# Kernel optimization log

Measured on AMD Instinct MI355X. Metric: run time of the kernel, lower is better.

The kernel has to match this reference:

```python
import jax, jax.numpy as jnp
import numpy as np

S, B, E = 1024, 64, 1024   # src_seq_len, batch, encoder_hidden_size
H, A = 1024, 1024          # decoder hidden, attention dim
EMB, V = 512, 32000        # embedding_dim, output vocab


def setup_inputs() -> dict:
    key = jax.random.key(0)
    ks = jax.random.split(key, 16)
    sd = lambda n: 1.0 / np.sqrt(n)
    u = lambda k, shape, n: jax.random.uniform(k, shape, jnp.float32, -sd(n), sd(n))
    return {
        "prev_y": jax.random.normal(ks[0], (B, EMB), jnp.float32),
        "prev_h": jax.random.normal(ks[1], (1, B, H), jnp.float32),
        "enc_out": jax.random.normal(ks[2], (S, B, E), jnp.float32),
        # attention params
        "U_w": u(ks[3], (A, E), E), "U_b": u(ks[4], (A,), E),
        "W_w": u(ks[5], (A, H), H), "W_b": u(ks[6], (A,), H),
        "v_w": u(ks[7], (1, A), A), "v_b": u(ks[8], (1,), A),
        # combine + GRU + output params
        "Wc_w": u(ks[9], (H, EMB + E), EMB + E), "Wc_b": u(ks[10], (H,), EMB + E),
        "W_ih": u(ks[11], (3 * H, H), H), "W_hh": u(ks[12], (3 * H, H), H),
        "b_ih": u(ks[13], (3 * H,), H), "b_hh": u(ks[14], (3 * H,), H),
        "Wout_w": u(ks[15], (V, H), H), "Wout_b": jnp.zeros((V,), jnp.float32),
        "mask": 768,
    }


def reference(prev_y, prev_h, enc_out, U_w, U_b, W_w, W_b, v_w, v_b,
              Wc_w, Wc_b, W_ih, W_hh, b_ih, b_hh, Wout_w, Wout_b, mask):
    s, b, e = enc_out.shape
    h = prev_h[0]                                     # [B,H]
    # --- additive (Bahdanau) attention with multiplicative 0/1 prefix mask ---
    uh = jnp.einsum('sbe,ae->sba', enc_out, U_w) + U_b  # [S,B,A]
    wq = h @ W_w.T + W_b                                # [B,A]
    scores = (jnp.tanh(uh + wq) @ v_w[0] + v_b[0]).T    # [B,S]
    m = min(int(mask), s)
    mask_vec = (jnp.arange(s) < m).astype(scores.dtype) # [S]
    scores = scores * mask_vec                          # multiply, NOT -inf (faithful)
    attn = jax.nn.softmax(scores, axis=1)               # [B,S]
    ctx = jnp.einsum('bs,sbe->be', attn, enc_out)       # [B,E]
    # --- combine + single GRU step (PyTorch gate order r,z,n) ---
    x = jnp.concatenate([prev_y, ctx], axis=1) @ Wc_w.T + Wc_b  # [B,H]
    gi = x @ W_ih.T + b_ih                              # [B,3H]
    gh = h @ W_hh.T + b_hh
    Hh = h.shape[1]
    r = jax.nn.sigmoid(gi[:, :Hh] + gh[:, :Hh])
    z = jax.nn.sigmoid(gi[:, Hh:2 * Hh] + gh[:, Hh:2 * Hh])
    n = jnp.tanh(gi[:, 2 * Hh:] + r * gh[:, 2 * Hh:])
    h_new = (1.0 - z) * n + z * h                       # [B,H]
    # --- output projection + log-softmax ---
    logits = h_new @ Wout_w.T + Wout_b                  # [B,V]
    dec_output = jax.nn.log_softmax(logits, axis=1)
    return dec_output, h_new[None], attn
```

## Files before the change

### kernel.cpp

```cpp
#include <hip/hip_runtime.h>

typedef float f32x4 __attribute__((ext_vector_type(4)));
typedef short short8 __attribute__((ext_vector_type(8)));
typedef unsigned int u32;

#define SEQ   1024
#define VOCAB 32000

__device__ __forceinline__ unsigned short f2bf(float f){
  union { float f; unsigned u; } v; v.f = f;
  unsigned r = v.u + 0x7FFFu + ((v.u >> 16) & 1u);
  return (unsigned short)(r >> 16);
}
__device__ __forceinline__ unsigned pk2(float a, float b){
  return (unsigned)f2bf(a) | ((unsigned)f2bf(b) << 16);
}
__device__ __forceinline__ float bf2f(unsigned short h){
  union { unsigned u; float f; } v; v.u = ((unsigned)h) << 16; return v.f;
}
__device__ __forceinline__ float tanh_fast(float x){
  float a = fminf(fmaxf(x, -15.f), 15.f);
  float e = __expf(2.f * a);
  return (e - 1.f) / (e + 1.f);
}
__device__ __forceinline__ float sigm(float x){ return 1.f / (1.f + expf(-x)); }

__device__ __forceinline__ void ld4(float4* dst, const float* p){
  const float4* q = (const float4*)p;
  dst[0]=q[0]; dst[1]=q[1]; dst[2]=q[2]; dst[3]=q[3];
}
__device__ __forceinline__ void cvt_store(char* base, int row, int kb0, const float4* f){
  int xs = (row & 7) << 4;
  uint4 u;
  u.x = pk2(f[0].x, f[0].y); u.y = pk2(f[0].z, f[0].w);
  u.z = pk2(f[1].x, f[1].y); u.w = pk2(f[1].z, f[1].w);
  *(uint4*)(base + row*128 + (kb0 ^ xs)) = u;
  u.x = pk2(f[2].x, f[2].y); u.y = pk2(f[2].z, f[2].w);
  u.z = pk2(f[3].x, f[3].y); u.w = pk2(f[3].z, f[3].w);
  *(uint4*)(base + row*128 + ((kb0 + 16) ^ xs)) = u;
}
__device__ __forceinline__ void gload_lds16(const void* g, void* l){
  __builtin_amdgcn_global_load_lds((const __attribute__((address_space(1))) u32*)g,
                                   (__attribute__((address_space(3))) u32*)l, 16, 0, 0);
}

__global__ __launch_bounds__(256)
void convert_all(const float* __restrict__ uw, const float* __restrict__ enc,
                 unsigned short* __restrict__ uwb, unsigned short* __restrict__ encb)
{
  const int UWC = 131072;
  const int TOT = UWC + 8388608;
  int stride = gridDim.x * 256;
  for (int c = blockIdx.x*256 + threadIdx.x; c < TOT; c += stride){
    const float* src; unsigned short* dst;
    if (c < UWC){ src = uw + (size_t)c*8;        dst = uwb + (size_t)c*8; }
    else        { size_t e = (size_t)(c-UWC)*8;  src = enc + e; dst = encb + e; }
    float4 f0 = ((const float4*)src)[0], f1 = ((const float4*)src)[1];
    uint4 u;
    u.x = pk2(f0.x,f0.y); u.y = pk2(f0.z,f0.w);
    u.z = pk2(f1.x,f1.y); u.w = pk2(f1.z,f1.w);
    *(uint4*)dst = u;
  }
}

__global__ __launch_bounds__(256)
void score_gemm_bf16(const unsigned short* __restrict__ encb,
                     const unsigned short* __restrict__ uwb,
                     const float* __restrict__ Ub, const float* __restrict__ vw,
                     const float* __restrict__ wqm, const int* __restrict__ maskp,
                     float* __restrict__ scores_part)
{
  __shared__ char smem[32768];
  int m = *maskp; m = m < 0 ? 0 : (m > SEQ ? SEQ : m);
  int bI = blockIdx.x;
  int mtile = bI & 511, ntile = bI >> 9;
  if (mtile * 2 >= m) return;
  int t = threadIdx.x, lane = t & 63, wid = t >> 6;
  int wm = wid >> 1, wn = wid & 1;

  int cswz = (((lane & 7) ^ (lane >> 3)) << 4);
  const char* pa = (const char*)encb + ((size_t)(mtile*128 + wid*8 + (lane>>3)))*2048 + cswz;
  const char* pb = (const char*)uwb  + ((size_t)(ntile*128 + wid*8 + (lane>>3)))*2048 + cswz;

  int aAddr[4], bAddr[4], aXor[4], bXor[4];
  #pragma unroll
  for (int i = 0; i < 4; ++i){
    int ra = wm*64 + i*16 + (lane & 15);
    aAddr[i] = ra * 128; aXor[i] = (ra & 7) << 4;
    int rb = wn*64 + i*16 + (lane & 15);
    bAddr[i] = rb * 128; bXor[i] = (rb & 7) << 4;
  }
  int klane = (lane >> 4) << 4;

  f32x4 acc[4][4] = {};
  char* bA = smem; char* bB = smem + 16384;

  for (int ks = 0; ks < 16; ++ks){
    __syncthreads();
    #pragma unroll
    for (int i = 0; i < 4; ++i){
      gload_lds16(pa + (size_t)i*65536 + ks*128, bA + (i*4 + wid)*1024);
      gload_lds16(pb + (size_t)i*65536 + ks*128, bB + (i*4 + wid)*1024);
    }
    __syncthreads();
    #pragma unroll
    for (int kk = 0; kk < 2; ++kk){
      short8 af[4], bv[4];
      int kb = kk * 64 + klane;
      #pragma unroll
      for (int i = 0; i < 4; ++i){
        af[i] = *(const short8*)(bA + aAddr[i] + (kb ^ aXor[i]));
        bv[i] = *(const short8*)(bB + bAddr[i] + (kb ^ bXor[i]));
      }
      #pragma unroll
      for (int mi = 0; mi < 4; ++mi)
        #pragma unroll
        for (int ni = 0; ni < 4; ++ni)
          acc[mi][ni] = __builtin_amdgcn_mfma_f32_16x16x32_bf16(af[mi], bv[ni], acc[mi][ni], 0, 0, 0);
    }
  }

  int s_idx = mtile * 2 + wm;
  if (s_idx < m){
    float ubv[4], vwv[4];
    #pragma unroll
    for (int ni = 0; ni < 4; ++ni){
      int nt = ntile*128 + wn*64 + ni*16 + (lane & 15);
      ubv[ni] = Ub[nt]; vwv[ni] = vw[nt];
    }
    #pragma unroll
    for (int mi = 0; mi < 4; ++mi){
      #pragma unroll
      for (int j = 0; j < 4; ++j){
        int b = mi*16 + ((lane >> 4) << 2) + j;
        const float* wqrow = wqm + b * 1024;
        float asum = 0.f;
        #pragma unroll
        for (int ni = 0; ni < 4; ++ni){
          int nt = ntile*128 + wn*64 + ni*16 + (lane & 15);
          float uh = acc[mi][ni][j] + ubv[ni] + wqrow[nt];
          asum += tanh_fast(uh) * vwv[ni];
        }
        asum += __shfl_xor(asum, 1, 64);
        asum += __shfl_xor(asum, 2, 64);
        asum += __shfl_xor(asum, 4, 64);
        asum += __shfl_xor(asum, 8, 64);
        if ((lane & 15) == 0)
          scores_part[(ntile*2 + wn)*65536 + s_idx*64 + b] = asum;
      }
    }
  }
}

__global__ __launch_bounds__(256, 2)
void score_gemm_f32(const float* __restrict__ enc, const float* __restrict__ Uw,
                    const float* __restrict__ Ub, const float* __restrict__ vw,
                    const float* __restrict__ wqm, const int* __restrict__ maskp,
                    float* __restrict__ scores_part)
{
  __shared__ char smem[65536];
  int m = *maskp; m = m < 0 ? 0 : (m > SEQ ? SEQ : m);
  int bI = blockIdx.x;
  int mtile = bI & 511, ntile = bI >> 9;
  if (mtile * 2 >= m) return;
  int row0 = mtile * 128;
  int t = threadIdx.x, lane = t & 63;
  int wid = t >> 6, wm = wid >> 1, wn = wid & 1;
  int srow = t >> 2;
  int sk4 = (t & 3) << 4;
  int kb0 = (t & 3) << 5;

  const float* Ag0 = enc + (size_t)(row0 + srow) * 1024 + sk4;
  const float* Ag1 = Ag0 + 64 * 1024;
  const float* Bg0 = Uw  + (size_t)(ntile * 128 + srow) * 1024 + sk4;
  const float* Bg1 = Bg0 + 64 * 1024;

  float4 fa0[4], fa1[4], fb0[4], fb1[4];
  int aAddr[4], bAddr[4], aXor[4], bXor[4];
  #pragma unroll
  for (int i = 0; i < 4; ++i){
    int ra = wm*64 + i*16 + (lane & 15);
    aAddr[i] = ra * 128; aXor[i] = (ra & 7) << 4;
    int rb = wn*64 + i*16 + (lane & 15);
    bAddr[i] = rb * 128; bXor[i] = (rb & 7) << 4;
  }
  int klane = (lane >> 4) << 4;
  f32x4 acc[4][4] = {};

  ld4(fa0, Ag0); ld4(fa1, Ag1); ld4(fb0, Bg0); ld4(fb1, Bg1);
  {
    char* bA = smem; char* bB = smem + 16384;
    cvt_store(bA, srow,      kb0, fa0);
    cvt_store(bA, srow + 64, kb0, fa1);
    cvt_store(bB, srow,      kb0, fb0);
    cvt_store(bB, srow + 64, kb0, fb1);
  }
  #pragma unroll 2
  for (int ks = 0; ks < 16; ++ks){
    int buf = ks & 1;
    if (ks < 15){
      int ko = (ks + 1) * 64;
      ld4(fa0, Ag0 + ko); ld4(fa1, Ag1 + ko);
      ld4(fb0, Bg0 + ko); ld4(fb1, Bg1 + ko);
    }
    __syncthreads();
    {
      char* bA = smem + buf * 32768;
      char* bB = bA + 16384;
      #pragma unroll
      for (int kk = 0; kk < 2; ++kk){
        short8 af[4], bv[4];
        int kb = kk * 64 + klane;
        #pragma unroll
        for (int i = 0; i < 4; ++i){
          af[i] = *(const short8*)(bA + aAddr[i] + (kb ^ aXor[i]));
          bv[i] = *(const short8*)(bB + bAddr[i] + (kb ^ bXor[i]));
        }
        #pragma unroll
        for (int mi = 0; mi < 4; ++mi)
          #pragma unroll
          for (int ni = 0; ni < 4; ++ni)
            acc[mi][ni] = __builtin_amdgcn_mfma_f32_16x16x32_bf16(af[mi], bv[ni], acc[mi][ni], 0, 0, 0);
      }
    }
    if (ks < 15){
      int nb = buf ^ 1;
      char* bA = smem + nb * 32768; char* bB = bA + 16384;
      cvt_store(bA, srow,      kb0, fa0);
      cvt_store(bA, srow + 64, kb0, fa1);
      cvt_store(bB, srow,      kb0, fb0);
      cvt_store(bB, srow + 64, kb0, fb1);
    }
  }

  int s_idx = mtile * 2 + wm;
  if (s_idx < m){
    float ubv[4], vwv[4];
    #pragma unroll
    for (int ni = 0; ni < 4; ++ni){
      int nt = ntile*128 + wn*64 + ni*16 + (lane & 15);
      ubv[ni] = Ub[nt]; vwv[ni] = vw[nt];
    }
    #pragma unroll
    for (int mi = 0; mi < 4; ++mi){
      #pragma unroll
      for (int j = 0; j < 4; ++j){
        int b = mi*16 + ((lane >> 4) << 2) + j;
        const float* wqrow = wqm + b * 1024;
        float asum = 0.f;
        #pragma unroll
        for (int ni = 0; ni < 4; ++ni){
          int nt = ntile*128 + wn*64 + ni*16 + (lane & 15);
          float uh = acc[mi][ni][j] + ubv[ni] + wqrow[nt];
          asum += tanh_fast(uh) * vwv[ni];
        }
        asum += __shfl_xor(asum, 1, 64);
        asum += __shfl_xor(asum, 2, 64);
        asum += __shfl_xor(asum, 4, 64);
        asum += __shfl_xor(asum, 8, 64);
        if ((lane & 15) == 0)
          scores_part[(ntile*2 + wn)*65536 + s_idx*64 + b] = asum;
      }
    }
  }
}

__global__ __launch_bounds__(256)
void gemm_m64(const float* __restrict__ A, const float* __restrict__ Bw,
              const float* __restrict__ bias, float* __restrict__ C,
              float* __restrict__ Cpart, int N, int K, int stepsPerZ)
{
  __shared__ unsigned short sA[2][64 * 40];
  __shared__ unsigned short sB[2][128 * 40];
  int t = threadIdx.x, lane = t & 63, wid = t >> 6;
  int ntile = blockIdx.x, z = blockIdx.z;
  int arow = t >> 2, ak = (t & 3) * 8;
  int brow = t >> 1, bk = (t & 1) * 16;
  const float* Ap = A + (size_t)arow * K + ak + (size_t)z * stepsPerZ * 32;
  const float* Bp = Bw + (size_t)(ntile * 128 + brow) * K + bk + (size_t)z * stepsPerZ * 32;
  int klane = (lane >> 4) << 4;
  f32x4 acc[4][2] = {};
  float4 a0, a1, b0, b1, b2, b3;

  {
    const float4* pa = (const float4*)Ap;
    a0 = pa[0]; a1 = pa[1];
    const float4* pb = (const float4*)Bp;
    b0 = pb[0]; b1 = pb[1]; b2 = pb[2]; b3 = pb[3];
    uint4 u;
    u.x = pk2(a0.x,a0.y); u.y = pk2(a0.z,a0.w);
    u.z = pk2(a1.x,a1.y); u.w = pk2(a1.z,a1.w);
    *(uint4*)((char*)sA[0] + arow*80 + ak*2) = u;
    u.x = pk2(b0.x,b0.y); u.y = pk2(b0.z,b0.w);
    u.z = pk2(b1.x,b1.y); u.w = pk2(b1.z,b1.w);
    *(uint4*)((char*)sB[0] + brow*80 + bk*2) = u;
    u.x = pk2(b2.x,b2.y); u.y = pk2(b2.z,b2.w);
    u.z = pk2(b3.x,b3.y); u.w = pk2(b3.z,b3.w);
    *(uint4*)((char*)sB[0] + brow*80 + bk*2 + 16) = u;
  }

  for (int ks = 0; ks < stepsPerZ; ++ks){
    int buf = ks & 1;
    if (ks + 1 < stepsPerZ){
      int kg = (ks + 1) * 32;
      const float4* pa = (const float4*)(Ap + kg);
      a0 = pa[0]; a1 = pa[1];
      const float4* pb = (const float4*)(Bp + kg);
      b0 = pb[0]; b1 = pb[1]; b2 = pb[2]; b3 = pb[3];
    }
    __syncthreads();
    {
      short8 af[4], bv[2];
      #pragma unroll
      for (int mi = 0; mi < 4; ++mi)
        af[mi] = *(const short8*)((char*)sA[buf] + (mi*16 + (lane & 15))*80 + klane);
      #pragma unroll
      for (int ni = 0; ni < 2; ++ni)
        bv[ni] = *(const short8*)((char*)sB[buf] + (wid*32 + ni*16 + (lane & 15))*80 + klane);
      #pragma unroll
      for (int mi = 0; mi < 4; ++mi)
        #pragma unroll
        for (int ni = 0; ni < 2; ++ni)
          acc[mi][ni] = __builtin_amdgcn_mfma_f32_16x16x32_bf16(af[mi], bv[ni], acc[mi][ni], 0, 0, 0);
    }
    if (ks + 1 < stepsPerZ){
      int nb = buf ^ 1;
      uint4 u;
      u.x = pk2(a0.x,a0.y); u.y = pk2(a0.z,a0.w);
      u.z = pk2(a1.x,a1.y); u.w = pk2(a1.z,a1.w);
      *(uint4*)((char*)sA[nb] + arow*80 + ak*2) = u;
      u.x = pk2(b0.x,b0.y); u.y = pk2(b0.z,b0.w);
      u.z = pk2(b1.x,b1.y); u.w = pk2(b1.z,b1.w);
      *(uint4*)((char*)sB[nb] + brow*80 + bk*2) = u;
      u.x = pk2(b2.x,b2.y); u.y = pk2(b2.z,b2.w);
      u.z = pk2(b3.x,b3.y); u.w = pk2(b3.z,b3.w);
      *(uint4*)((char*)sB[nb] + brow*80 + bk*2 + 16) = u;
    }
  }

  bool multi = (gridDim.z > 1);
  #pragma unroll
  for (int ni = 0; ni < 2; ++ni){
    int cg = ntile*128 + wid*32 + ni*16 + (lane & 15);
    float bz = (bias && !multi) ? bias[cg] : 0.f;
    #pragma unroll
    for (int mi = 0; mi < 4; ++mi){
      int r0 = mi*16 + ((lane >> 4) << 2);
      #pragma unroll
      for (int j = 0; j < 4; ++j){
        float val = acc[mi][ni][j] + bz;
        if (multi) Cpart[((size_t)z*64 + r0 + j)*N + cg] = val;
        else       C[(size_t)(r0 + j)*N + cg] = val;
      }
    }
  }
}

__global__ __launch_bounds__(256)
void reduce8_bias(const float* __restrict__ part, const float* __restrict__ bias,
                  float* __restrict__ out, int N)
{
  int idx = blockIdx.x*256 + threadIdx.x;
  int r = idx / (N >> 2), c4 = (idx % (N >> 2)) * 4;
  f32x4 acc = *(const f32x4*)(bias + c4);
  #pragma unroll
  for (int z = 0; z < 8; ++z)
    acc += *(const f32x4*)(part + ((size_t)z*64 + r)*N + c4);
  *(f32x4*)(out + (size_t)r*N + c4) = acc;
}

__global__ __launch_bounds__(256)
void softmax_attn(const float* __restrict__ sp, const float* __restrict__ vb,
                  const int* __restrict__ maskp, float* __restrict__ attn)
{
  __shared__ float sb[4];
  int b = blockIdx.x, t = threadIdx.x, lane = t & 63, wid = t >> 6;
  int m = *maskp; m = m < 0 ? 0 : (m > SEQ ? SEQ : m);
  float vb0 = vb[0];
  float v[4]; float mx = -1e30f;
  #pragma unroll
  for (int k = 0; k < 4; ++k){
    int s = t + k * 256;
    float x = 0.f;
    if (s < m){
      float a = 0.f;
      #pragma unroll
      for (int p = 0; p < 16; ++p) a += sp[p*65536 + s*64 + b];
      x = a + vb0;
    }
    v[k] = x; mx = fmaxf(mx, x);
  }
  for (int d = 1; d < 64; d <<= 1) mx = fmaxf(mx, __shfl_xor(mx, d, 64));
  if (lane == 0) sb[wid] = mx;
  __syncthreads();
  mx = fmaxf(fmaxf(sb[0], sb[1]), fmaxf(sb[2], sb[3]));
  float sum = 0.f;
  #pragma unroll
  for (int k = 0; k < 4; ++k){ v[k] = expf(v[k] - mx); sum += v[k]; }
  for (int d = 1; d < 64; d <<= 1) sum += __shfl_xor(sum, d, 64);
  __syncthreads();
  if (lane == 0) sb[wid] = sum;
  __syncthreads();
  sum = sb[0] + sb[1] + sb[2] + sb[3];
  #pragma unroll
  for (int k = 0; k < 4; ++k) attn[b*1024 + t + k*256] = v[k] / sum;
}

__global__ __launch_bounds__(256)
void ctx_bf16(const float* __restrict__ attn, const unsigned short* __restrict__ encb,
              float* __restrict__ ctx_part)
{
  int b = blockIdx.x >> 4, ch = blockIdx.x & 15;
  int t = threadIdx.x;
  __shared__ float a_s[64];
  if (t < 64) a_s[t] = attn[b*1024 + ch*64 + t];
  __syncthreads();
  const unsigned short* base = encb + ((size_t)(ch*64)*64 + b)*1024 + t*4;
  f32x4 acc = {};
  for (int s2 = 0; s2 < 64; ++s2){
    ushort4 vv = *(const ushort4*)(base + (size_t)s2*65536);
    float w = a_s[s2];
    acc.x += w * bf2f(vv.x); acc.y += w * bf2f(vv.y);
    acc.z += w * bf2f(vv.z); acc.w += w * bf2f(vv.w);
  }
  *(f32x4*)(ctx_part + (size_t)(b*16 + ch)*1024 + t*4) = acc;
}

__global__ __launch_bounds__(256)
void ctx_f32(const float* __restrict__ attn, const float* __restrict__ enc,
             float* __restrict__ ctx_part)
{
  int b = blockIdx.x >> 4, ch = blockIdx.x & 15;
  int t = threadIdx.x;
  __shared__ float a_s[64];
  if (t < 64) a_s[t] = attn[b*1024 + ch*64 + t];
  __syncthreads();
  const float* ep = enc + (size_t)(ch * 64) * 65536 + b * 1024 + t * 4;
  f32x4 acc = {};
  for (int s2 = 0; s2 < 64; ++s2){
    f32x4 v = *(const f32x4*)(ep + (size_t)s2 * 65536);
    acc += a_s[s2] * v;
  }
  *(f32x4*)(ctx_part + (size_t)(b*16 + ch)*1024 + t*4) = acc;
}

__global__ __launch_bounds__(256)
void build_xcat(const float* __restrict__ part, const float* __restrict__ py,
                float* __restrict__ xcat)
{
  int b = blockIdx.x, t = threadIdx.x;
  f32x4 acc = {};
  #pragma unroll
  for (int c2 = 0; c2 < 16; ++c2)
    acc += *(const f32x4*)(part + (size_t)(b*16 + c2) * 1024 + t * 4);
  *(f32x4*)(xcat + b*1536 + 512 + t*4) = acc;
  if (t < 128)
    *(f32x4*)(xcat + b*1536 + t*4) = *(const f32x4*)(py + b*512 + t*4);
}

__global__ __launch_bounds__(256)
void gru_fused(const float* __restrict__ gip, const float* __restrict__ ghp,
               const float* __restrict__ b_ih, const float* __restrict__ b_hh,
               const float* __restrict__ h, float* __restrict__ hnew)
{
  int idx = blockIdx.x * 256 + threadIdx.x;
  int b = idx >> 10, i = idx & 1023;
  float gr = b_ih[i], gz = b_ih[1024+i], gn = b_ih[2048+i];
  float hr = b_hh[i], hz = b_hh[1024+i], hn = b_hh[2048+i];
  #pragma unroll
  for (int z = 0; z < 8; ++z){
    const float* p = gip + (size_t)z*196608 + b*3072;
    gr += p[i]; gz += p[1024+i]; gn += p[2048+i];
    const float* q = ghp + (size_t)z*196608 + b*3072;
    hr += q[i]; hz += q[1024+i]; hn += q[2048+i];
  }
  float r  = sigm(gr + hr);
  float zz = sigm(gz + hz);
  float n  = tanhf(gn + r * hn);
  hnew[idx] = (1.f - zz) * n + zz * h[idx];
}

__global__ __launch_bounds__(1024)
void logsoftmax_kernel(float* __restrict__ logits)
{
  __shared__ float sb[16];
  int b = blockIdx.x, t = threadIdx.x, lane = t & 63, wid = t >> 6;
  float* row = logits + (size_t)b * VOCAB;
  float v[32]; float mx = -1e30f;
  #pragma unroll
  for (int k = 0; k < 32; ++k){
    int idx = t + k * 1024;
    if (idx < VOCAB){ v[k] = row[idx]; mx = fmaxf(mx, v[k]); }
    else v[k] = -1e30f;
  }
  for (int d = 1; d < 64; d <<= 1) mx = fmaxf(mx, __shfl_xor(mx, d, 64));
  if (lane == 0) sb[wid] = mx;
  __syncthreads();
  float m2 = -1e30f;
  for (int i = 0; i < 16; ++i) m2 = fmaxf(m2, sb[i]);
  mx = m2;
  float sum = 0.f;
  #pragma unroll
  for (int k = 0; k < 32; ++k){
    int idx = t + k * 1024;
    if (idx < VOCAB) sum += expf(v[k] - mx);
  }
  for (int d = 1; d < 64; d <<= 1) sum += __shfl_xor(sum, d, 64);
  __syncthreads();
  if (lane == 0) sb[wid] = sum;
  __syncthreads();
  float s2 = 0.f;
  for (int i = 0; i < 16; ++i) s2 += sb[i];
  float lse = mx + logf(s2);
  #pragma unroll
  for (int k = 0; k < 32; ++k){
    int idx = t + k * 1024;
    if (idx < VOCAB) row[idx] = v[k] - lse;
  }
}

extern "C" void kernel_launch(void* const* d_in, const int* in_sizes, int n_in,
                              void* d_out, int out_size, void* d_ws, size_t ws_size,
                              hipStream_t stream)
{
  const float* prev_y = (const float*)d_in[0];
  const float* prev_h = (const float*)d_in[1];
  const float* enc    = (const float*)d_in[2];
  const float* U_w    = (const float*)d_in[3];
  const float* U_b    = (const float*)d_in[4];
  const float* W_w    = (const float*)d_in[5];
  const float* W_b    = (const float*)d_in[6];
  const float* v_w    = (const float*)d_in[7];
  const float* v_b    = (const float*)d_in[8];
  const float* Wc_w   = (const float*)d_in[9];
  const float* Wc_b   = (const float*)d_in[10];
  const float* W_ih   = (const float*)d_in[11];
  const float* W_hh   = (const float*)d_in[12];
  const float* b_ih   = (const float*)d_in[13];
  const float* b_hh   = (const float*)d_in[14];
  const float* Wout_w = (const float*)d_in[15];
  const float* Wout_b = (const float*)d_in[16];
  const int*   maskp  = (const int*)d_in[17];

  char* wsb = (char*)d_ws;
  const size_t ENC_B = 134217728ULL;
  const size_t UW_B  = 2097152ULL;
  const size_t FLOATS_B = 26083328ULL;
  bool big = ws_size >= ENC_B + UW_B + FLOATS_B;

  unsigned short* encb = (unsigned short*)wsb;
  unsigned short* uwb  = (unsigned short*)(wsb + ENC_B);
  float* f = (float*)(wsb + (big ? (ENC_B + UW_B) : 0));
  float* scores_part = f;
  float* wq_part     = scores_part + 1048576;
  float* wq          = wq_part + 524288;
  float* ctx_part    = wq + 65536;
  float* xcat        = ctx_part + 1048576;
  float* xvec_part   = xcat + 98304;
  float* xvec        = xvec_part + 524288;
  float* gi_part     = xvec + 65536;
  float* gh_part     = gi_part + 1572864;

  float* out_logp = (float*)d_out;
  float* out_h    = out_logp + 64 * VOCAB;
  float* out_attn = out_h + 65536;

  if (big)
    convert_all<<<2048, 256, 0, stream>>>(U_w, enc, uwb, encb);

  gemm_m64<<<dim3(8,1,8), 256, 0, stream>>>(prev_h, W_w, nullptr, nullptr, wq_part, 1024, 1024, 4);
  reduce8_bias<<<64, 256, 0, stream>>>(wq_part, W_b, wq, 1024);

  if (big)
    score_gemm_bf16<<<4096, 256, 0, stream>>>(encb, uwb, U_b, v_w, wq, maskp, scores_part);
  else
    score_gemm_f32<<<4096, 256, 0, stream>>>(enc, U_w, U_b, v_w, wq, maskp, scores_part);

  softmax_attn<<<64, 256, 0, stream>>>(scores_part, v_b, maskp, out_attn);

  if (big) ctx_bf16<<<1024, 256, 0, stream>>>(out_attn, encb, ctx_part);
  else     ctx_f32<<<1024, 256, 0, stream>>>(out_attn, enc, ctx_part);
  build_xcat<<<64, 256, 0, stream>>>(ctx_part, prev_y, xcat);

  gemm_m64<<<dim3(8,1,8), 256, 0, stream>>>(xcat, Wc_w, nullptr, nullptr, xvec_part, 1024, 1536, 6);
  reduce8_bias<<<64, 256, 0, stream>>>(xvec_part, Wc_b, xvec, 1024);

  gemm_m64<<<dim3(24,1,8), 256, 0, stream>>>(xvec, W_ih, nullptr, nullptr, gi_part, 3072, 1024, 4);
  gemm_m64<<<dim3(24,1,8), 256, 0, stream>>>(prev_h, W_hh, nullptr, nullptr, gh_part, 3072, 1024, 4);
  gru_fused<<<256, 256, 0, stream>>>(gi_part, gh_part, b_ih, b_hh, prev_h, out_h);

  gemm_m64<<<dim3(250,1,1), 256, 0, stream>>>(out_h, Wout_w, Wout_b, out_logp, nullptr, VOCAB, 1024, 32);
  logsoftmax_kernel<<<64, 1024, 0, stream>>>(out_logp);
}
```

Baseline: 806.3 us.

## Double-buffer LDS loads in bf16 score GEMM and transpose partial-score layout

The bf16 score GEMM now double-buffers its shared-memory tiles (64KB). It issues the next k-step's global-to-LDS loads before computing on the current buffer and uses vmcnt waits with raw barriers, so load latency can overlap with MFMA work. Separately, the partial-score buffer layout changes from [s][b] to [b][s], which makes the softmax reads over s coalesced. The larger LDS footprint may reduce occupancy.

```diff
diff --git a/kernel.cpp b/kernel.cpp
--- a/kernel.cpp
+++ b/kernel.cpp
@@ -70,7 +70,7 @@
                      const float* __restrict__ wqm, const int* __restrict__ maskp,
                      float* __restrict__ scores_part)
 {
-  __shared__ char smem[32768];
+  __shared__ char smem[65536];
   int m = *maskp; m = m < 0 ? 0 : (m > SEQ ? SEQ : m);
   int bI = blockIdx.x;
   int mtile = bI & 511, ntile = bI >> 9;
@@ -91,33 +91,51 @@
     bAddr[i] = rb * 128; bXor[i] = (rb & 7) << 4;
   }
   int klane = (lane >> 4) << 4;
+  int ldsDst = wid * 1024;
 
   f32x4 acc[4][4] = {};
-  char* bA = smem; char* bB = smem + 16384;
-
-  for (int ks = 0; ks < 16; ++ks){
-    __syncthreads();
+
+  {
+    char* bA = smem; char* bB = smem + 16384;
     #pragma unroll
     for (int i = 0; i < 4; ++i){
-      gload_lds16(pa + (size_t)i*65536 + ks*128, bA + (i*4 + wid)*1024);
-      gload_lds16(pb + (size_t)i*65536 + ks*128, bB + (i*4 + wid)*1024);
-    }
-    __syncthreads();
-    #pragma unroll
-    for (int kk = 0; kk < 2; ++kk){
-      short8 af[4], bv[4];
-      int kb = kk * 64 + klane;
+      gload_lds16(pa + (size_t)i*65536, bA + i*4096 + ldsDst);
+      gload_lds16(pb + (size_t)i*65536, bB + i*4096 + ldsDst);
+    }
+  }
+
+  for (int ks = 0; ks < 16; ++ks){
+    if (ks < 15){
+      char* bA = smem + ((ks+1)&1)*32768; char* bB = bA + 16384;
       #pragma unroll
       for (int i = 0; i < 4; ++i){
-        af[i] = *(const short8*)(bA + aAddr[i] + (kb ^ aXor[i]));
-        bv[i] = *(const short8*)(bB + bAddr[i] + (kb ^ bXor[i]));
+        gload_lds16(pa + (size_t)i*65536 + (ks+1)*128, bA + i*4096 + ldsDst);
+        gload_lds16(pb + (size_t)i*65536 + (ks+1)*128, bB + i*4096 + ldsDst);
       }
-      #pragma unroll
-      for (int mi = 0; mi < 4; ++mi)
+      asm volatile("s_waitcnt vmcnt(8)" ::: "memory");
+    } else {
+      asm volatile("s_waitcnt vmcnt(0)" ::: "memory");
+    }
+    __builtin_amdgcn_s_barrier();
+    {
+      char* bA = smem + (ks&1)*32768; char* bB = bA + 16384;
+      #pragma unroll
+      for (int kk = 0; kk < 2; ++kk){
+        short8 af[4], bv[4];
+        int kb = kk * 64 + klane;
         #pragma unroll
-        for (int ni = 0; ni < 4; ++ni)
-          acc[mi][ni] = __builtin_amdgcn_mfma_f32_16x16x32_bf16(af[mi], bv[ni], acc[mi][ni], 0, 0, 0);
-    }
+        for (int i = 0; i < 4; ++i){
+          af[i] = *(const short8*)(bA + aAddr[i] + (kb ^ aXor[i]));
+          bv[i] = *(const short8*)(bB + bAddr[i] + (kb ^ bXor[i]));
+        }
+        #pragma unroll
+        for (int mi = 0; mi < 4; ++mi)
+          #pragma unroll
+          for (int ni = 0; ni < 4; ++ni)
+            acc[mi][ni] = __builtin_amdgcn_mfma_f32_16x16x32_bf16(af[mi], bv[ni], acc[mi][ni], 0, 0, 0);
+      }
+    }
+    __builtin_amdgcn_s_barrier();
   }
 
   int s_idx = mtile * 2 + wm;
@@ -146,7 +164,7 @@
         asum += __shfl_xor(asum, 4, 64);
         asum += __shfl_xor(asum, 8, 64);
         if ((lane & 15) == 0)
-          scores_part[(ntile*2 + wn)*65536 + s_idx*64 + b] = asum;
+          scores_part[(ntile*2 + wn)*65536 + b*1024 + s_idx] = asum;
       }
     }
   }
@@ -259,7 +277,7 @@
         asum += __shfl_xor(asum, 4, 64);
         asum += __shfl_xor(asum, 8, 64);
         if ((lane & 15) == 0)
-          scores_part[(ntile*2 + wn)*65536 + s_idx*64 + b] = asum;
+          scores_part[(ntile*2 + wn)*65536 + b*1024 + s_idx] = asum;
       }
     }
   }
@@ -385,7 +403,7 @@
     if (s < m){
       float a = 0.f;
       #pragma unroll
-      for (int p = 0; p < 16; ++p) a += sp[p*65536 + s*64 + b];
+      for (int p = 0; p < 16; ++p) a += sp[p*65536 + b*1024 + s];
       x = a + vb0;
     }
     v[k] = x; mx = fmaxf(mx, x);
```

Result: faster. 763.6 us (-5.3%).
